# Kernel tuning notes

Measured on AMD Instinct MI355X. Metric: run time of the kernel, lower is better.

## Reference

```python
import jax, jax.numpy as jnp
import numpy as np

EPS = 1e-6

def safe_softmax(x, axis=-1):
    x_max = jnp.max(x, axis=axis, keepdims=True)
    x_exp = jnp.exp(x - x_max)
    return x_exp / (jnp.sum(x_exp, axis=axis, keepdims=True) + EPS)

def setup_inputs() -> dict:
    key = jax.random.key(0)
    ks = jax.random.split(key, 8)
    B, S, D = 16, 2048, 1024
    scale = 1.0 / np.sqrt(D)
    x = jax.random.normal(ks[0], (B, S, D), dtype=jnp.float32)
    y = jax.random.normal(ks[1], (B, S, D), dtype=jnp.float32)
    Wq = jax.random.normal(ks[2], (D, D), dtype=jnp.float32) * scale
    bq = jnp.zeros((D,), dtype=jnp.float32)
    Wk = jax.random.normal(ks[3], (D, D), dtype=jnp.float32) * scale
    bk = jnp.zeros((D,), dtype=jnp.float32)
    Wv = jax.random.normal(ks[4], (D, D), dtype=jnp.float32) * scale
    bv = jnp.zeros((D,), dtype=jnp.float32)
    return {"x": x, "y": y, "Wq": Wq, "bq": bq, "Wk": Wk, "bk": bk, "Wv": Wv, "bv": bv}

def reference(x, y, Wq, bq, Wk, bk, Wv, bv):
    # Q/K/V projections: [B, S, D]
    Q = jnp.einsum('bsd,df->bsf', x, Wq) + bq
    K = jnp.einsum('bsd,df->bsf', y, Wk) + bk
    V = jnp.einsum('bsd,df->bsf', y, Wv) + bv
    D = K.shape[-1]
    # single-head attention over full [B, Sq, Skv] score matrix
    logits = jnp.einsum('bqd,bkd->bqk', Q, K) / jnp.sqrt(jnp.float32(D))
    attn = safe_softmax(logits, axis=-1)
    out = jnp.einsum('bqk,bkd->bqd', attn, V)
    return out + x
```

## Files before the change

### kernel.cpp

```cpp
#include <hip/hip_runtime.h>
#include <hip/hip_bf16.h>

typedef __attribute__((ext_vector_type(8))) short bf16x8;
typedef __attribute__((ext_vector_type(4))) float f32x4;
typedef __attribute__((ext_vector_type(2))) long i64x2;

__device__ __forceinline__ float bf2f(short u) {
  union { unsigned int u; float f; } c;
  c.u = ((unsigned int)(unsigned short)u) << 16;
  return c.f;
}
__device__ __forceinline__ short f2bf(float f) {
  union { float f; unsigned int u; } c; c.f = f;
  unsigned int r = (c.u + 0x7fffu + ((c.u >> 16) & 1u)) >> 16;
  return (short)(unsigned short)r;
}

__device__ __forceinline__ float fp8_dec(unsigned b) {
  union { unsigned u; float f; } c;
  c.u = (b & 0x7fu) << 20;
  float v = c.f * 1.329227995784916e+36f;
  return (b & 0x80u) ? -v : v;
}

__device__ __forceinline__ void gload16(const void* g, void* l) {
  __builtin_amdgcn_global_load_lds(
      (const __attribute__((address_space(1))) unsigned int*)g,
      (__attribute__((address_space(3))) unsigned int*)l, 16, 0, 0);
}

__device__ __forceinline__ int fp8_g(int s) {
  return (s >> 6) * 64 + ((s >> 3) & 3) * 16 + ((s >> 5) & 1) * 8 + (s & 7);
}

__global__ __launch_bounds__(256) void cvt2_k(const float* __restrict__ x,
                                              const float* __restrict__ y,
                                              short* __restrict__ xb,
                                              short* __restrict__ yb, int n4) {
  const float* in = blockIdx.z ? y : x;
  short* out = blockIdx.z ? yb : xb;
  int i = blockIdx.x * blockDim.x + threadIdx.x;
  const int stride = gridDim.x * blockDim.x;
  for (; i < n4; i += stride) {
    float4 v = ((const float4*)in)[i];
    short4 o;
    o.x = f2bf(v.x); o.y = f2bf(v.y); o.z = f2bf(v.z); o.w = f2bf(v.w);
    ((short4*)out)[i] = o;
  }
}

__global__ __launch_bounds__(256) void cvtT3_k(
    const float* __restrict__ Wq, const float* __restrict__ Wk,
    const float* __restrict__ Wv, short* __restrict__ Wqt,
    short* __restrict__ Wkt, short* __restrict__ Wvt) {
  const float* W = (blockIdx.z == 0) ? Wq : (blockIdx.z == 1) ? Wk : Wv;
  short* Wt = (blockIdx.z == 0) ? Wqt : (blockIdx.z == 1) ? Wkt : Wvt;
  __shared__ float tile[32][33];
  const int n0 = blockIdx.x * 32, k0 = blockIdx.y * 32;
  const int tr = threadIdx.x >> 5;
  const int tc = threadIdx.x & 31;
#pragma unroll
  for (int p = 0; p < 4; ++p)
    tile[p * 8 + tr][tc] = W[(long long)(k0 + p * 8 + tr) * 1024 + n0 + tc];
  __syncthreads();
#pragma unroll
  for (int p = 0; p < 4; ++p)
    Wt[(long long)(n0 + p * 8 + tr) * 1024 + k0 + tc] = f2bf(tile[tc][p * 8 + tr]);
}


#define STG6(sp, ld8, dOff) do { \
  gload16((sp), Ls + (dOff)); \
  gload16((const char*)(sp) + (ld8), Ls + (dOff) + 512); } while (0)

#define RD_A6(BUF, QM) do { \
  _Pragma("unroll") \
  for (int mi = 0; mi < 4; ++mi) { \
    aR[mi][0] = *(const bf16x8*)(Ls + (BUF) + (QM)*8192 + arow + mi*1024 + aO0); \
    aR[mi][1] = *(const bf16x8*)(Ls + (BUF) + (QM)*8192 + arow + mi*1024 + aO1); \
  } } while (0)

#define RD_B6(DST, BUF, QN) do { \
  _Pragma("unroll") \
  for (int ni = 0; ni < 2; ++ni) { \
    DST[ni][0] = *(const bf16x8*)(Ls + (BUF) + 16384 + (QN)*8192 + brow + ni*1024 + aO0); \
    DST[ni][1] = *(const bf16x8*)(Ls + (BUF) + 16384 + (QN)*8192 + brow + ni*1024 + aO1); \
  } } while (0)

#define SYNCIN6 do { \
  __builtin_amdgcn_sched_barrier(0); \
  __builtin_amdgcn_s_barrier(); \
  asm volatile("s_waitcnt lgkmcnt(0)" ::: "memory"); \
  __builtin_amdgcn_sched_barrier(0); \
  __builtin_amdgcn_s_setprio(1); } while (0)

#define SYNCOUT6 do { \
  __builtin_amdgcn_s_setprio(0); \
  __builtin_amdgcn_s_barrier(); } while (0)

#define MF166(ACCQ, BB) do { \
  _Pragma("unroll") \
  for (int mi = 0; mi < 4; ++mi) { \
    _Pragma("unroll") \
    for (int ni = 0; ni < 2; ++ni) { \
      ACCQ[mi][ni] = __builtin_amdgcn_mfma_f32_16x16x32_bf16(aR[mi][0], BB[ni][0], ACCQ[mi][ni], 0, 0, 0); \
      ACCQ[mi][ni] = __builtin_amdgcn_mfma_f32_16x16x32_bf16(aR[mi][1], BB[ni][1], ACCQ[mi][ni], 0, 0, 0); \
    } \
  } } while (0)

template<int EPI>
__global__ __launch_bounds__(512) void gemm256_k(
    const short* __restrict__ A, const short* __restrict__ Bt,
    void* __restrict__ Cv, const float* __restrict__ X,
    const float* __restrict__ X2,
    int K, int lda, int ldb, int ldc,
    long long strA, long long strB, long long strC) {
  __shared__ __align__(16) short Ls[65536];

  const int lane = threadIdx.x & 63;
  const int w = threadIdx.x >> 6;
  const int wm = w >> 2, wn = w & 3;
  const int w1k = w * 1024;
  const int l15 = lane & 15;
  const int g4 = lane >> 4;
  const int p8 = lane & 7;
  const int r8 = lane >> 3;
  const int aO0 = (g4 ^ p8) << 3;
  const int aO1 = ((4 + g4) ^ p8) << 3;
  const int arow = (wm * 64 + l15) * 64;
  const int brow = (wn * 32 + l15) * 64;

  const int gx = gridDim.x, gy = gridDim.y;
  const int nwg = gx * gy * gridDim.z;
  int lid = blockIdx.x + gx * (blockIdx.y + gy * blockIdx.z);
  lid = (lid & 7) * (nwg >> 3) + (lid >> 3);
  const int bx = lid % gx;
  const int rem = lid / gx;
  const int by = rem % gy;
  const int bz = rem / gy;

  const int n0 = bx * 256;
  const int m0 = by * 256;
  const int nt = K >> 6;
  const int nit = nt >> 1;

  const float* Xs = bz ? X2 : X;

  const long long ldaB = 2LL * lda, ldbB = 2LL * ldb;
  const long long ldaB8 = 8 * ldaB, ldbB8 = 8 * ldbB;
  const long long hOffA = 128 * ldaB, hOffB = 128 * ldbB;

  const char* pA = (const char*)(A + bz * strA)
      + (long long)(m0 + w * 16 + r8) * ldaB + ((p8 ^ r8) << 4);
  const char* pB = (const char*)(Bt + bz * strB)
      + (long long)(n0 + w * 16 + r8) * ldbB + ((p8 ^ r8) << 4);

  f32x4 acc[2][2][4][2] = {};
  bf16x8 aR[4][2], bR0[2][2], bR1[2][2];

  STG6(pA,                 ldaB8, 0 + w1k);
  STG6(pA + hOffA,         ldaB8, 8192 + w1k);
  STG6(pB,                 ldbB8, 16384 + w1k);
  STG6(pB + hOffB,         ldbB8, 24576 + w1k);
  STG6(pA + 128,           ldaB8, 32768 + w1k);
  STG6(pA + 128 + hOffA,   ldaB8, 40960 + w1k);
  STG6(pB + 128,           ldbB8, 49152 + w1k);
  STG6(pB + 128 + hOffB,   ldbB8, 57344 + w1k);
  asm volatile("s_waitcnt vmcnt(8)" ::: "memory");
  __builtin_amdgcn_s_barrier();

  for (int j = 0; j < nit; ++j) {
    const bool st = (j + 1 < nit);

    RD_A6(0, 0); RD_B6(bR0, 0, 0);
    SYNCIN6; MF166(acc[0][0], bR0); SYNCOUT6;
    RD_B6(bR1, 0, 1);
    if (st) { STG6(pA + 256, ldaB8, 0 + w1k);
              STG6(pB + 256, ldbB8, 16384 + w1k); }
    SYNCIN6; MF166(acc[0][1], bR1); SYNCOUT6;
    RD_A6(0, 1);
    if (st) STG6(pB + 256 + hOffB, ldbB8, 24576 + w1k);
    SYNCIN6; MF166(acc[1][1], bR1); SYNCOUT6;
    if (st) STG6(pA + 256 + hOffA, ldaB8, 8192 + w1k);
    SYNCIN6; MF166(acc[1][0], bR0);
    __builtin_amdgcn_s_setprio(0);
    if (st) asm volatile("s_waitcnt vmcnt(8)" ::: "memory");
    else    asm volatile("s_waitcnt vmcnt(0)" ::: "memory");
    __builtin_amdgcn_s_barrier();

    RD_A6(32768, 0); RD_B6(bR0, 32768, 0);
    SYNCIN6; MF166(acc[0][0], bR0); SYNCOUT6;
    RD_B6(bR1, 32768, 1);
    if (st) { STG6(pA + 384, ldaB8, 32768 + w1k);
              STG6(pB + 384, ldbB8, 49152 + w1k); }
    SYNCIN6; MF166(acc[0][1], bR1); SYNCOUT6;
    RD_A6(32768, 1);
    if (st) STG6(pB + 384 + hOffB, ldbB8, 57344 + w1k);
    SYNCIN6; MF166(acc[1][1], bR1); SYNCOUT6;
    if (st) STG6(pA + 384 + hOffA, ldaB8, 40960 + w1k);
    SYNCIN6; MF166(acc[1][0], bR0);
    __builtin_amdgcn_s_setprio(0);
    if (st) asm volatile("s_waitcnt vmcnt(8)" ::: "memory");
    __builtin_amdgcn_s_barrier();

    pA += 256; pB += 256;
  }

  const int rB = g4 * 4;
  if (EPI == 3) {
    unsigned char* C = (unsigned char*)Cv;
#pragma unroll
    for (int qn = 0; qn < 2; ++qn)
#pragma unroll
      for (int ni = 0; ni < 2; ++ni) {
        const int col = n0 + qn * 128 + wn * 32 + ni * 16 + l15;
        const int b2 = col >> 11;
        const int s = col & 2047;
        const int gs = fp8_g(s);
#pragma unroll
        for (int qm = 0; qm < 2; ++qm)
#pragma unroll
          for (int mi = 0; mi < 4; ++mi)
#pragma unroll
            for (int r = 0; r < 4; ++r) {
              const int row = m0 + qm * 128 + wm * 64 + mi * 16 + rB + r;
              const float v = acc[qm][qn][mi][ni][r] + Xs[row];
              const unsigned d = __builtin_amdgcn_cvt_pk_fp8_f32(v, v, 0, false);
              C[(long long)b2 * 2097152 + (long long)row * 2048 + gs] =
                  (unsigned char)(d & 0xff);
            }
      }
  } else {
    unsigned char* C = (unsigned char*)Cv + bz * strC;
#pragma unroll
    for (int qn = 0; qn < 2; ++qn)
#pragma unroll
      for (int ni = 0; ni < 2; ++ni) {
        const int col = n0 + qn * 128 + wn * 32 + ni * 16 + l15;
        const int gs = fp8_g(col);
        const float bv = Xs[col];
#pragma unroll
        for (int qm = 0; qm < 2; ++qm)
#pragma unroll
          for (int mi = 0; mi < 4; ++mi)
#pragma unroll
            for (int r = 0; r < 4; ++r) {
              const int row = m0 + qm * 128 + wm * 64 + mi * 16 + rB + r;
              const float v = acc[qm][qn][mi][ni][r] + bv;
              const unsigned d = __builtin_amdgcn_cvt_pk_fp8_f32(v, v, 0, false);
              C[(long long)row * ldc + gs] = (unsigned char)(d & 0xff);
            }
      }
  }
}

__global__ __launch_bounds__(256) void softmax8_k(const unsigned char* __restrict__ Sl8,
                                                  unsigned char* __restrict__ P8) {
  __shared__ float redm[4];
  __shared__ float reds[4];
  const long long row = blockIdx.x;
  const unsigned char* p = Sl8 + row * 2048;
  const int t = threadIdx.x;
  const int w = t >> 6, lane = t & 63;
  const unsigned long long v8 = *(const unsigned long long*)(p + t * 8);
  float f[8];
  float mx = -3.0e38f;
#pragma unroll
  for (int j = 0; j < 8; ++j) {
    f[j] = fp8_dec((unsigned)(v8 >> (8 * j)) & 0xffu);
    mx = fmaxf(mx, f[j]);
  }
#pragma unroll
  for (int o = 32; o > 0; o >>= 1) mx = fmaxf(mx, __shfl_xor(mx, o));
  if (lane == 0) redm[w] = mx;
  __syncthreads();
  mx = fmaxf(fmaxf(redm[0], redm[1]), fmaxf(redm[2], redm[3]));
  float s = 0.f;
#pragma unroll
  for (int j = 0; j < 8; ++j) { f[j] = __expf(f[j] - mx); s += f[j]; }
#pragma unroll
  for (int o = 32; o > 0; o >>= 1) s += __shfl_xor(s, o);
  if (lane == 0) reds[w] = s;
  __syncthreads();
  s = reds[0] + reds[1] + reds[2] + reds[3];
  const float inv = 256.0f / (s + 1e-6f);
  unsigned d0 = __builtin_amdgcn_cvt_pk_fp8_f32(f[0] * inv, f[1] * inv, 0, false);
  d0 = __builtin_amdgcn_cvt_pk_fp8_f32(f[2] * inv, f[3] * inv, d0, true);
  unsigned d1 = __builtin_amdgcn_cvt_pk_fp8_f32(f[4] * inv, f[5] * inv, 0, false);
  d1 = __builtin_amdgcn_cvt_pk_fp8_f32(f[6] * inv, f[7] * inv, d1, true);
  const int grp = t >> 3, pc = t & 7;
  unsigned char* dst = P8 + row * 2048 + grp * 64 + (pc & 3) * 16 + (pc >> 2) * 8;
  *(unsigned long long*)dst =
      (unsigned long long)d0 | ((unsigned long long)d1 << 32);
}


template<int EPI>
__global__ __launch_bounds__(512, 4) void g8fp8_k(
    const unsigned char* __restrict__ A8, const unsigned char* __restrict__ B8,
    void* __restrict__ Cv, const float* __restrict__ X,
    int K, int ldaB, int ldbB, int ldc,
    long long strA, long long strB, long long strC, long long strX, float scale) {
  __shared__ __align__(16) char Ls[73728];

  const int lane = threadIdx.x & 63;
  const int w = threadIdx.x >> 6;
  const int wm = w >> 1, wn = w & 1;
  const int l15 = lane & 15;
  const int g4 = lane >> 4;
  const int swB = ((g4 ^ ((l15 >> 1) & 3)) << 4);
  const int arow = (wm * 64 + l15) * 64 + swB;
  const int brow = (wn * 64 + l15) * 64 + swB;
  const int sg = (lane & 3) ^ ((lane >> 3) & 3);

  const int gx = gridDim.x, gy = gridDim.y;
  const int nwg = gx * gy * gridDim.z;
  int lid = blockIdx.x + gx * (blockIdx.y + gy * blockIdx.z);
  lid = (lid & 7) * (nwg >> 3) + (lid >> 3);
  const int bx = lid % gx;
  const int rem = lid / gx;
  const int by = rem % gy;
  const int bz = rem / gy;
  const int n0 = bx * 128, m0 = by * 256;
  const int nt = K >> 6;

  const long long ldaL = ldaB, ldbL = ldbB;
  const char* pA = (const char*)A8 + bz * strA
      + (long long)(m0 + w * 32 + (lane >> 2)) * ldaL + sg * 16;
  const char* pB = (const char*)B8 + bz * strB
      + (long long)(n0 + w * 16 + (lane >> 2)) * ldbL + sg * 16;
  const long long ldaL16 = 16 * ldaL;

  char* dA = Ls + w * 2048;
  char* dB = Ls + 16384 + w * 1024;

  f32x4 acc[4][4] = {};

#pragma unroll
  for (int i = 0; i < 3; ++i) {
    const char* qA = pA + i * 64;
    gload16(qA,           dA + i * 24576);
    gload16(qA + ldaL16,  dA + i * 24576 + 1024);
    gload16(pB + i * 64,  dB + i * 24576);
  }
  asm volatile("s_waitcnt vmcnt(6)" ::: "memory");
  __builtin_amdgcn_s_barrier();

  int cur = 0;
  for (int t = 0; t < nt; ++t) {
    const int bufO = cur * 24576;
    i64x2 aA[4], bB[4];
#pragma unroll
    for (int mi = 0; mi < 4; ++mi)
      aA[mi] = *(const i64x2*)(Ls + bufO + arow + mi * 1024);
#pragma unroll
    for (int ni = 0; ni < 4; ++ni)
      bB[ni] = *(const i64x2*)(Ls + bufO + 16384 + brow + ni * 1024);
    asm volatile("s_waitcnt lgkmcnt(0)" ::: "memory");
    __builtin_amdgcn_s_barrier();
    if (t + 3 < nt) {
      const char* qA = pA + (t + 3) * 64;
      gload16(qA,          dA + bufO);
      gload16(qA + ldaL16, dA + bufO + 1024);
      gload16(pB + (t + 3) * 64, dB + bufO);
    }
    __builtin_amdgcn_sched_barrier(0);
    __builtin_amdgcn_s_setprio(1);
#pragma unroll
    for (int mi = 0; mi < 4; ++mi)
#pragma unroll
      for (int ni = 0; ni < 4; ++ni) {
        acc[mi][ni] = __builtin_amdgcn_mfma_f32_16x16x32_fp8_fp8(
            aA[mi][0], bB[ni][0], acc[mi][ni], 0, 0, 0);
        acc[mi][ni] = __builtin_amdgcn_mfma_f32_16x16x32_fp8_fp8(
            aA[mi][1], bB[ni][1], acc[mi][ni], 0, 0, 0);
      }
    __builtin_amdgcn_s_setprio(0);
    if (t + 3 < nt)      asm volatile("s_waitcnt vmcnt(6)" ::: "memory");
    else if (t + 2 < nt) asm volatile("s_waitcnt vmcnt(3)" ::: "memory");
    else                 asm volatile("s_waitcnt vmcnt(0)" ::: "memory");
    __builtin_amdgcn_s_barrier();
    cur = (cur == 2) ? 0 : cur + 1;
  }

  const int rB = g4 * 4;
  if (EPI == 1) {
    unsigned char* C = (unsigned char*)Cv + bz * strC;
#pragma unroll
    for (int ni = 0; ni < 4; ++ni) {
      const int col = n0 + wn * 64 + ni * 16 + l15;
#pragma unroll
      for (int mi = 0; mi < 4; ++mi)
#pragma unroll
        for (int r = 0; r < 4; ++r) {
          const int row = m0 + wm * 64 + mi * 16 + rB + r;
          const float v = acc[mi][ni][r] * scale;
          const unsigned d = __builtin_amdgcn_cvt_pk_fp8_f32(v, v, 0, false);
          C[(long long)row * ldc + col] = (unsigned char)(d & 0xff);
        }
    }
  } else {
    float* C = (float*)Cv + bz * strC;
    const float* Xb = X + bz * strX;
#pragma unroll
    for (int ni = 0; ni < 4; ++ni) {
      const int col = n0 + wn * 64 + ni * 16 + l15;
#pragma unroll
      for (int mi = 0; mi < 4; ++mi)
#pragma unroll
        for (int r = 0; r < 4; ++r) {
          const int row = m0 + wm * 64 + mi * 16 + rB + r;
          const long long idx = (long long)row * ldc + col;
          C[idx] = acc[mi][ni][r] * scale + Xb[idx];
        }
    }
  }
}

extern "C" void kernel_launch(void* const* d_in, const int* in_sizes, int n_in,
                              void* d_out, int out_size, void* d_ws, size_t ws_size,
                              hipStream_t stream) {
  const float* x  = (const float*)d_in[0];
  const float* y  = (const float*)d_in[1];
  const float* Wq = (const float*)d_in[2];
  const float* bq = (const float*)d_in[3];
  const float* Wk = (const float*)d_in[4];
  const float* bk = (const float*)d_in[5];
  const float* Wv = (const float*)d_in[6];
  const float* bv = (const float*)d_in[7];
  float* out = (float*)d_out;

  const long long SD  = 2048LL * 1024;
  const long long BSD = 16LL * SD;
  const long long SS  = 2048LL * 2048;

  char* ws = (char*)d_ws;
  short* xb  = (short*)ws;
  short* yb  = xb + BSD;
  unsigned char* Sl8 = (unsigned char*)ws;
  unsigned char* Q8 = (unsigned char*)(ws + 134217728);
  unsigned char* K8 = (unsigned char*)(ws + 167772160);
  unsigned char* P8 = Q8;
  unsigned char* V8 = (unsigned char*)(ws + 268435456);
  short* Wqt = (short*)(ws + 335544320);
  short* Wkt = Wqt + 1024 * 1024;
  short* Wvt = Wkt + 1024 * 1024;

  cvt2_k<<<dim3(2048, 1, 2), 256, 0, stream>>>(x, y, xb, yb, (int)(BSD / 4));

  cvtT3_k<<<dim3(32, 32, 3), 256, 0, stream>>>(Wq, Wk, Wv, Wqt, Wkt, Wvt);

  gemm256_k<4><<<dim3(4, 128, 2), 512, 0, stream>>>(
      xb, Wqt, Q8, bq, bk, 1024, 1024, 1024, 1024,
      BSD, 1048576LL, 33554432LL);

  gemm256_k<3><<<dim3(128, 4, 1), 512, 0, stream>>>(
      Wvt, yb, V8, bv, nullptr, 1024, 1024, 1024, 0, 0, 0, 0);

  g8fp8_k<1><<<dim3(16, 8, 16), 512, 0, stream>>>(
      Q8, K8, Sl8, nullptr, 1024, 1024, 1024, 2048,
      2097152LL, 2097152LL, SS, 0, 0.03125f);

  softmax8_k<<<32768, 256, 0, stream>>>(Sl8, P8);

  g8fp8_k<2><<<dim3(8, 8, 16), 512, 0, stream>>>(
      P8, V8, out, x, 2048, 2048, 2048, 1024,
      4194304LL, 2097152LL, SD, SD, 0.00390625f);

  (void)in_sizes; (void)n_in; (void)out_size; (void)ws_size;
}
```

Before: 602.4 us.

## Enlarge fp8 attention GEMM tile to 256x256 with 16-wave workgroups

Widens the fp8 GEMM tile used for QK^T and PV from 256x128 to 256x256, using 1024-thread workgroups of 16 waves arranged 4x4. Half the waves load the A tile and half load the B tile, so each wave issues two loads per stage and the vmcnt waits are adjusted to match. The larger tile raises arithmetic intensity and cuts redundant global reads. In exchange it uses 96KB of LDS per block, which lowers occupancy, and launches half as many workgroups.

```diff
diff --git a/kernel.cpp b/kernel.cpp
--- a/kernel.cpp
+++ b/kernel.cpp
@@ -296,16 +296,16 @@
 
 
 template<int EPI>
-__global__ __launch_bounds__(512, 4) void g8fp8_k(
+__global__ __launch_bounds__(1024, 4) void g8x256_k(
     const unsigned char* __restrict__ A8, const unsigned char* __restrict__ B8,
     void* __restrict__ Cv, const float* __restrict__ X,
     int K, int ldaB, int ldbB, int ldc,
     long long strA, long long strB, long long strC, long long strX, float scale) {
-  __shared__ __align__(16) char Ls[73728];
+  __shared__ __align__(16) char Ls[98304];
 
   const int lane = threadIdx.x & 63;
   const int w = threadIdx.x >> 6;
-  const int wm = w >> 1, wn = w & 1;
+  const int wm = w >> 2, wn = w & 3;
   const int l15 = lane & 15;
   const int g4 = lane >> 4;
   const int swB = ((g4 ^ ((l15 >> 1) & 3)) << 4);
@@ -321,34 +321,33 @@
   const int rem = lid / gx;
   const int by = rem % gy;
   const int bz = rem / gy;
-  const int n0 = bx * 128, m0 = by * 256;
+  const int n0 = bx * 256, m0 = by * 256;
   const int nt = K >> 6;
 
   const long long ldaL = ldaB, ldbL = ldbB;
-  const char* pA = (const char*)A8 + bz * strA
-      + (long long)(m0 + w * 32 + (lane >> 2)) * ldaL + sg * 16;
-  const char* pB = (const char*)B8 + bz * strB
-      + (long long)(n0 + w * 16 + (lane >> 2)) * ldbL + sg * 16;
-  const long long ldaL16 = 16 * ldaL;
-
-  char* dA = Ls + w * 2048;
-  char* dB = Ls + 16384 + w * 1024;
+  const bool isA = (w < 8);
+  const int wS = isA ? w : (w - 8);
+  const char* pS = isA
+      ? ((const char*)A8 + bz * strA
+         + (long long)(m0 + wS * 32 + (lane >> 2)) * ldaL + sg * 16)
+      : ((const char*)B8 + bz * strB
+         + (long long)(n0 + wS * 32 + (lane >> 2)) * ldbL + sg * 16);
+  const long long ld16S = 16 * (isA ? ldaL : ldbL);
+  char* dS = Ls + (isA ? 0 : 16384) + wS * 2048;
 
   f32x4 acc[4][4] = {};
 
 #pragma unroll
   for (int i = 0; i < 3; ++i) {
-    const char* qA = pA + i * 64;
-    gload16(qA,           dA + i * 24576);
-    gload16(qA + ldaL16,  dA + i * 24576 + 1024);
-    gload16(pB + i * 64,  dB + i * 24576);
-  }
-  asm volatile("s_waitcnt vmcnt(6)" ::: "memory");
+    gload16(pS + i * 64,         dS + i * 32768);
+    gload16(pS + i * 64 + ld16S, dS + i * 32768 + 1024);
+  }
+  asm volatile("s_waitcnt vmcnt(4)" ::: "memory");
   __builtin_amdgcn_s_barrier();
 
   int cur = 0;
   for (int t = 0; t < nt; ++t) {
-    const int bufO = cur * 24576;
+    const int bufO = cur * 32768;
     i64x2 aA[4], bB[4];
 #pragma unroll
     for (int mi = 0; mi < 4; ++mi)
@@ -359,10 +358,8 @@
     asm volatile("s_waitcnt lgkmcnt(0)" ::: "memory");
     __builtin_amdgcn_s_barrier();
     if (t + 3 < nt) {
-      const char* qA = pA + (t + 3) * 64;
-      gload16(qA,          dA + bufO);
-      gload16(qA + ldaL16, dA + bufO + 1024);
-      gload16(pB + (t + 3) * 64, dB + bufO);
+      gload16(pS + (t + 3) * 64,         dS + bufO);
+      gload16(pS + (t + 3) * 64 + ld16S, dS + bufO + 1024);
     }
     __builtin_amdgcn_sched_barrier(0);
     __builtin_amdgcn_s_setprio(1);
@@ -376,8 +373,8 @@
             aA[mi][1], bB[ni][1], acc[mi][ni], 0, 0, 0);
       }
     __builtin_amdgcn_s_setprio(0);
-    if (t + 3 < nt)      asm volatile("s_waitcnt vmcnt(6)" ::: "memory");
-    else if (t + 2 < nt) asm volatile("s_waitcnt vmcnt(3)" ::: "memory");
+    if (t + 3 < nt)      asm volatile("s_waitcnt vmcnt(4)" ::: "memory");
+    else if (t + 2 < nt) asm volatile("s_waitcnt vmcnt(2)" ::: "memory");
     else                 asm volatile("s_waitcnt vmcnt(0)" ::: "memory");
     __builtin_amdgcn_s_barrier();
     cur = (cur == 2) ? 0 : cur + 1;
@@ -457,13 +454,13 @@
   gemm256_k<3><<<dim3(128, 4, 1), 512, 0, stream>>>(
       Wvt, yb, V8, bv, nullptr, 1024, 1024, 1024, 0, 0, 0, 0);
 
-  g8fp8_k<1><<<dim3(16, 8, 16), 512, 0, stream>>>(
+  g8x256_k<1><<<dim3(8, 8, 16), 1024, 0, stream>>>(
       Q8, K8, Sl8, nullptr, 1024, 1024, 1024, 2048,
       2097152LL, 2097152LL, SS, 0, 0.03125f);
 
   softmax8_k<<<32768, 256, 0, stream>>>(Sl8, P8);
 
-  g8fp8_k<2><<<dim3(8, 8, 16), 512, 0, stream>>>(
+  g8x256_k<2><<<dim3(4, 8, 16), 1024, 0, stream>>>(
       P8, V8, out, x, 2048, 2048, 2048, 1024,
       4194304LL, 2097152LL, SD, SD, 0.00390625f);
 
```

New measurement: 627.8 us. 4.2% more time.
